# Kernel tuning notes

Hardware: AMD Instinct MI355X
Metric: run time of the kernel (lower is better)

## Reference

```python
import jax, jax.numpy as jnp
import numpy as np

B, N, C = 16, 32768, 3
PRE, POST, IOU_THRESH = 4096, 512, 0.7


def setup_inputs() -> dict:
    key = jax.random.key(0)
    k1, k2, k3, k4 = jax.random.split(key, 4)
    centers = jax.random.uniform(k1, (B, N, 3), minval=0.0, maxval=70.0)
    sizes = jax.random.uniform(k2, (B, N, 3), minval=1.0, maxval=5.0)
    ry = jax.random.uniform(k3, (B, N, 1), minval=-np.pi, maxval=np.pi)
    batch_box_preds = jnp.concatenate([centers, sizes, ry], axis=-1)  # (B,N,7)
    batch_cls_preds = jax.random.uniform(k4, (B, N, C))  # normalized class scores
    return {"batch_box_preds": batch_box_preds, "batch_cls_preds": batch_cls_preds}


def _nms_single(boxes, scores):
    """Greedy class-agnostic NMS for one sample.
    boxes: (N,7) [x,y,z,dx,dy,dz,ry]; scores: (N,).
    Returns selected indices into the original N boxes and a validity mask,
    both of fixed length POST (padded).
    BEV IoU uses axis-aligned footprints (x,y,dx,dy)."""
    top_s, top_i = jax.lax.top_k(scores, PRE)  # pre-maxsize filtering by score
    tb = boxes[top_i]  # (PRE,7)
    x1 = tb[:, 0] - tb[:, 3] * 0.5
    x2 = tb[:, 0] + tb[:, 3] * 0.5
    y1 = tb[:, 1] - tb[:, 4] * 0.5
    y2 = tb[:, 1] + tb[:, 4] * 0.5
    area = (x2 - x1) * (y2 - y1)

    def step(active, _):
        ms = jnp.where(active, top_s, -jnp.inf)
        j = jnp.argmax(ms)
        valid = active[j]
        ix = jnp.clip(jnp.minimum(x2, x2[j]) - jnp.maximum(x1, x1[j]), 0.0)
        iy = jnp.clip(jnp.minimum(y2, y2[j]) - jnp.maximum(y1, y1[j]), 0.0)
        inter = ix * iy
        iou = inter / (area + area[j] - inter + 1e-8)
        # suppress overlapping boxes (j suppresses itself, iou==1)
        active = active & jnp.where(valid, iou < IOU_THRESH, True)
        return active, (jnp.where(valid, top_i[j], 0), valid)

    active0 = jnp.ones(PRE, dtype=bool)
    _, (sel_idx, sel_valid) = jax.lax.scan(step, active0, None, length=POST)
    return sel_idx, sel_valid


def reference(batch_box_preds, batch_cls_preds):
    # cur_roi_scores, cur_roi_labels = torch.max(cls_preds, dim=1)
    scores = jnp.max(batch_cls_preds, axis=-1)          # (B,N)
    labels = jnp.argmax(batch_cls_preds, axis=-1)       # (B,N)
    sel_idx, sel_valid = jax.vmap(_nms_single)(batch_box_preds, scores)  # (B,POST)
    gather = jax.vmap(lambda a, i: a[i])
    rois = jnp.where(sel_valid[..., None], gather(batch_box_preds, sel_idx), 0.0)  # (B,POST,7)
    roi_scores = jnp.where(sel_valid, gather(scores, sel_idx), 0.0)                # (B,POST)
    roi_labels = jnp.where(sel_valid, gather(labels, sel_idx), 0) + 1              # (B,POST), pad -> 1 as in torch code
    return rois, roi_scores, roi_labels
```

## Files before the change

kernel.cpp:

```cpp
#include <hip/hip_runtime.h>
#include <stdint.h>

#define BATCH 16
#define NBOX  32768
#define PRE   4096
#define POST  512

typedef unsigned long long u64;
typedef unsigned int u32;

__device__ inline u64 shfl64(u64 v, int src) {
    int lo = __shfl((int)(v & 0xffffffffULL), src);
    int hi = __shfl((int)(v >> 32), src);
    return ((u64)(u32)hi << 32) | (u32)lo;
}

__global__ __launch_bounds__(1024) void k_sortkeys4096(const float* __restrict__ cls,
                                                       u64* __restrict__ out) {
    __shared__ u64 s[PRE];
    int g = blockIdx.x;
    u64* dst = out + (size_t)g * PRE;
    int tid = threadIdx.x;
    for (int i = tid; i < PRE; i += 1024) {
        int idx = g * PRE + i;
        const float* c = cls + (size_t)idx * 3;
        float sc = fmaxf(fmaxf(c[0], c[1]), c[2]);
        u32 sb = __float_as_uint(sc);
        s[i] = ((u64)(~sb) << 32) | (u32)(idx & (NBOX - 1));
    }
    for (int k = 2; k <= PRE; k <<= 1) {
        for (int jj = k >> 1; jj > 0; jj >>= 1) {
            __syncthreads();
            for (int p = tid; p < PRE / 2; p += 1024) {
                int i = 2 * p - (p & (jj - 1));
                int l = i + jj;
                bool asc = ((i & k) == 0);
                u64 a = s[i], b = s[l];
                if ((a > b) == asc) { s[i] = b; s[l] = a; }
            }
        }
    }
    __syncthreads();
    for (int i = tid; i < PRE; i += 1024) dst[i] = s[i];
}

__global__ __launch_bounds__(1024) void k_merge(const u64* __restrict__ in,
                                                u64* __restrict__ out, int npairs) {
    __shared__ u64 s[PRE];
    int b = blockIdx.x / npairs, p = blockIdx.x % npairs;
    const u64* A  = in + ((size_t)b * npairs * 2 + (size_t)p * 2) * PRE;
    const u64* Bp = A + PRE;
    u64* dst = out + ((size_t)b * npairs + p) * PRE;
    int tid = threadIdx.x;
    for (int i = tid; i < PRE; i += 1024) {
        u64 a = A[i], bb = Bp[PRE - 1 - i];
        s[i] = a < bb ? a : bb;
    }
    for (int jj = PRE / 2; jj > 0; jj >>= 1) {
        __syncthreads();
        for (int p2 = tid; p2 < PRE / 2; p2 += 1024) {
            int i = 2 * p2 - (p2 & (jj - 1));
            int l = i + jj;
            u64 a = s[i], bb = s[l];
            if (a > bb) { s[i] = bb; s[l] = a; }
        }
    }
    __syncthreads();
    for (int i = tid; i < PRE; i += 1024) dst[i] = s[i];
}

__global__ __launch_bounds__(256) void k_coords(const u64* __restrict__ topkeys,
                                                const float* __restrict__ boxes,
                                                float* __restrict__ cx1,
                                                float* __restrict__ cy1,
                                                float* __restrict__ cx2,
                                                float* __restrict__ cy2,
                                                float* __restrict__ car,
                                                u64* __restrict__ flags) {
    int g = blockIdx.x * 256 + threadIdx.x;
    if (g < BATCH * 64) flags[g] = 0ULL;
    int b = g >> 12;
    u64 key = topkeys[g];
    int n = (int)(key & 0xffffffffULL);
    const float* bp = boxes + ((size_t)b * NBOX + n) * 7;
    float cx = bp[0], cy = bp[1], dx = bp[3], dy = bp[4];
    float hx = __fmul_rn(dx, 0.5f), hy = __fmul_rn(dy, 0.5f);
    float x1 = __fsub_rn(cx, hx), x2 = __fadd_rn(cx, hx);
    float y1 = __fsub_rn(cy, hy), y2 = __fadd_rn(cy, hy);
    cx1[g] = x1; cy1[g] = y1; cx2[g] = x2; cy2[g] = y2;
    car[g] = __fmul_rn(__fsub_rn(x2, x1), __fsub_rn(y2, y1));
}

__global__ __launch_bounds__(256) void k_iou(const float* __restrict__ cx1,
                                             const float* __restrict__ cy1,
                                             const float* __restrict__ cx2,
                                             const float* __restrict__ cy2,
                                             const float* __restrict__ car,
                                             u64* __restrict__ maskp,
                                             u64* __restrict__ flags) {
    __shared__ float s1[64], s2[64], s3[64], s4[64], s5[64];
    int b = blockIdx.y;
    int t = blockIdx.x, blk = 0;
    while (t >= 64 - blk) { t -= 64 - blk; ++blk; }
    int wd = blk + t;
    size_t base = (size_t)b * PRE;
    int tid = threadIdx.x;
    if (tid < 64) {
        int i = blk * 64 + tid;
        s1[tid] = cx1[base + i]; s2[tid] = cy1[base + i];
        s3[tid] = cx2[base + i]; s4[tid] = cy2[base + i];
        s5[tid] = car[base + i];
    }
    __syncthreads();
    int w = tid >> 6, lane = tid & 63;
    int j = wd * 64 + lane;
    float jx1 = cx1[base + j], jy1 = cy1[base + j];
    float jx2 = cx2[base + j], jy2 = cy2[base + j];
    float ja  = car[base + j];
    const double M = (double)0.7f - 0x1p-25;
    u64 wavebits = 0;
    int r0 = w * 16;
    #pragma unroll 4
    for (int r = 0; r < 16; ++r) {
        int i = blk * 64 + r0 + r;
        float rx1 = s1[r0 + r], ry1 = s2[r0 + r];
        float rx2 = s3[r0 + r], ry2 = s4[r0 + r], ra = s5[r0 + r];
        float ix = fmaxf(__fsub_rn(fminf(jx2, rx2), fmaxf(jx1, rx1)), 0.0f);
        float iy = fmaxf(__fsub_rn(fminf(jy2, ry2), fmaxf(jy1, ry1)), 0.0f);
        float inter = __fmul_rn(ix, iy);
        bool cand = (j > i) && (inter > 0.0f);
        u64 m = 0;
        if (__ballot(cand)) {
            float ssum = __fadd_rn(ja, ra);
            float d    = __fsub_rn(ssum, inter);
            float q    = __fadd_rn(d, 1e-8f);
            bool sup = cand && ((double)inter > M * (double)q);
            m = __ballot(sup);
        }
        if (lane == 0) maskp[((base + i) << 6) + wd] = m;
        if (m) wavebits |= 1ULL << (r0 + r);
    }
    if (lane == 0 && wavebits)
        atomicOr((unsigned long long*)&flags[b * 64 + blk], wavebits);
}

__global__ __launch_bounds__(256) void k_walk(const u64* __restrict__ maskp,
                                              const u64* __restrict__ flagbits,
                                              const u64* __restrict__ topkeys,
                                              const float* __restrict__ boxes,
                                              const float* __restrict__ cls,
                                              float* __restrict__ out) {
    __shared__ int ssel[POST];
    __shared__ int scnt;
    int b = blockIdx.x;
    int tid = threadIdx.x;
    const u64* keys = topkeys + (size_t)b * PRE;

    if (tid < 64) {
        int lane = tid;
        u64 act = ~0ULL;
        u64 nzf = flagbits[b * 64 + lane];
        int cnt = 0;
        while (true) {
            u64 bal = __ballot(act != 0ULL);
            if (!bal) break;
            int fw = __ffsll(bal) - 1;
            u64 wsel = shfl64(act, fw);
            int i = (fw << 6) + __ffsll(wsel) - 1;
            if (lane == 0) ssel[cnt] = i;
            cnt++;
            if (cnt == POST) break;
            if (lane == fw) act &= ~(1ULL << (i & 63));
            u64 fword = shfl64(nzf, fw);
            if ((fword >> (i & 63)) & 1ULL) {
                u64 row = maskp[(((size_t)b * PRE + i) << 6) + lane];
                if (lane >= fw) act &= ~row;
            }
        }
        if (lane == 0) scnt = cnt;
    }
    __syncthreads();
    int cnt = scnt;
    for (int k = tid; k < POST; k += 256) if (k >= cnt) ssel[k] = -1;
    __syncthreads();

    const int R1 = BATCH * POST * 7;
    const int R2 = R1 + BATCH * POST;
    for (int k = tid; k < POST; k += 256) {
        int j = ssel[k];
        float* ro = out + ((size_t)b * POST + k) * 7;
        float score = 0.0f, labelf = 1.0f;
        if (j >= 0) {
            u64 key = keys[j];
            int n = (int)(key & 0xffffffffULL);
            const float* bp = boxes + ((size_t)b * NBOX + n) * 7;
            #pragma unroll
            for (int c = 0; c < 7; ++c) ro[c] = bp[c];
            score = __uint_as_float(~(u32)(key >> 32));
            const float* cp = cls + ((size_t)b * NBOX + n) * 3;
            float c0 = cp[0], c1 = cp[1], c2 = cp[2];
            int lab = 0; float best = c0;
            if (c1 > best) { best = c1; lab = 1; }
            if (c2 > best) { lab = 2; }
            labelf = (float)(lab + 1);
        } else {
            #pragma unroll
            for (int c = 0; c < 7; ++c) ro[c] = 0.0f;
        }
        out[R1 + b * POST + k] = score;
        out[R2 + b * POST + k] = labelf;
    }
}

__global__ __launch_bounds__(1024) void k_nms(const u64* __restrict__ topkeys,
                                              const float* __restrict__ boxes,
                                              const float* __restrict__ cls,
                                              float* __restrict__ out) {
    __shared__ float sx1[PRE], sy1[PRE], sx2[PRE], sy2[PRE], sarea[PRE];
    __shared__ int   sorig[PRE];
    __shared__ u64   smask[PRE / 64];
    __shared__ int   ssel[POST];
    __shared__ int   scur;
    int b = blockIdx.x;
    int tid = threadIdx.x;
    const u64* keys = topkeys + (size_t)b * PRE;

    for (int i = tid; i < PRE; i += 1024) {
        u64 key = keys[i];
        int n = (int)(key & 0xffffffffULL);
        sorig[i] = n;
        const float* bp = boxes + ((size_t)b * NBOX + n) * 7;
        float cx = bp[0], cy = bp[1], dx = bp[3], dy = bp[4];
        float hx = __fmul_rn(dx, 0.5f), hy = __fmul_rn(dy, 0.5f);
        float x1 = __fsub_rn(cx, hx), x2 = __fadd_rn(cx, hx);
        float y1 = __fsub_rn(cy, hy), y2 = __fadd_rn(cy, hy);
        sx1[i] = x1; sx2[i] = x2; sy1[i] = y1; sy2[i] = y2;
        sarea[i] = __fmul_rn(__fsub_rn(x2, x1), __fsub_rn(y2, y1));
    }
    if (tid < PRE / 64) smask[tid] = ~0ULL;
    __syncthreads();

    int lane = tid & 63;
    int wv   = tid >> 6;
    for (int r = 0; r < POST; ++r) {
        if (tid < 64) {
            u64 w = smask[lane];
            u64 nz = __ballot(w != 0ULL);
            int j = -1;
            if (nz) {
                int fw = __ffsll(nz) - 1;
                u64 wf = shfl64(w, fw);
                j = (fw << 6) + __ffsll(wf) - 1;
            }
            if (lane == 0) { scur = j; ssel[r] = j; }
        }
        __syncthreads();
        int j = scur;
        if (j < 0) {
            for (int k = r + tid; k < POST; k += 1024) ssel[k] = -1;
            __syncthreads();
            break;
        }
        float x1j = sx1[j], x2j = sx2[j], y1j = sy1[j], y2j = sy2[j], aj = sarea[j];
        for (int wd = wv * 4; wd < wv * 4 + 4; ++wd) {
            u64 m = smask[wd];
            if (m == 0ULL) continue;
            int i = (wd << 6) + lane;
            float ix = fmaxf(__fsub_rn(fminf(sx2[i], x2j), fmaxf(sx1[i], x1j)), 0.0f);
            float iy = fmaxf(__fsub_rn(fminf(sy2[i], y2j), fmaxf(sy1[i], y1j)), 0.0f);
            float inter = __fmul_rn(ix, iy);
            float denom = __fadd_rn(__fsub_rn(__fadd_rn(sarea[i], aj), inter), 1e-8f);
            float iou = __fdiv_rn(inter, denom);
            u64 clr = __ballot(!(iou < 0.7f));
            if (lane == 0) smask[wd] = m & ~clr;
        }
        __syncthreads();
    }

    const int R1 = BATCH * POST * 7;
    const int R2 = R1 + BATCH * POST;
    for (int k = tid; k < POST; k += 1024) {
        int j = ssel[k];
        float* ro = out + ((size_t)b * POST + k) * 7;
        float score = 0.0f, labelf = 1.0f;
        if (j >= 0) {
            int n = sorig[j];
            const float* bp = boxes + ((size_t)b * NBOX + n) * 7;
            #pragma unroll
            for (int c = 0; c < 7; ++c) ro[c] = bp[c];
            u64 key = keys[j];
            score = __uint_as_float(~(u32)(key >> 32));
            const float* cp = cls + ((size_t)b * NBOX + n) * 3;
            float c0 = cp[0], c1 = cp[1], c2 = cp[2];
            int lab = 0; float best = c0;
            if (c1 > best) { best = c1; lab = 1; }
            if (c2 > best) { lab = 2; }
            labelf = (float)(lab + 1);
        } else {
            #pragma unroll
            for (int c = 0; c < 7; ++c) ro[c] = 0.0f;
        }
        out[R1 + b * POST + k] = score;
        out[R2 + b * POST + k] = labelf;
    }
}

extern "C" void kernel_launch(void* const* d_in, const int* in_sizes, int n_in,
                              void* d_out, int out_size, void* d_ws, size_t ws_size,
                              hipStream_t stream) {
    const float* boxes = (const float*)d_in[0];
    const float* cls   = (const float*)d_in[1];
    float* out = (float*)d_out;

    char* ws = (char*)d_ws;
    u64*   keysA = (u64*)(ws + 0);
    u64*   keysB = (u64*)(ws + 4194304);
    float* cx1   = (float*)(ws + 8388608);
    float* cy1   = (float*)(ws + 8650752);
    float* cx2   = (float*)(ws + 8912896);
    float* cy2   = (float*)(ws + 9175040);
    float* car   = (float*)(ws + 9437184);
    u64*   flags = (u64*)(ws + 9699328);
    u64*   maskp = (u64*)(ws + 9707520);
    const size_t NEED = 9707520 + (size_t)BATCH * PRE * 64 * 8;

    k_sortkeys4096<<<BATCH * 8, 1024, 0, stream>>>(cls, keysB);
    k_merge<<<BATCH * 4, 1024, 0, stream>>>(keysB, keysA, 4);
    k_merge<<<BATCH * 2, 1024, 0, stream>>>(keysA, keysB, 2);

    if (ws_size >= NEED) {
        k_merge<<<BATCH, 1024, 0, stream>>>(keysB, keysA, 1);
        k_coords<<<(BATCH * PRE) / 256, 256, 0, stream>>>(keysA, boxes,
                                                          cx1, cy1, cx2, cy2, car, flags);
        k_iou<<<dim3(2080, BATCH), 256, 0, stream>>>(cx1, cy1, cx2, cy2, car,
                                                     maskp, flags);
        k_walk<<<BATCH, 256, 0, stream>>>(maskp, flags, keysA, boxes, cls, out);
    } else {
        k_merge<<<BATCH, 1024, 0, stream>>>(keysB, keysA, 1);
        k_nms<<<BATCH, 1024, 0, stream>>>(keysA, boxes, cls, out);
    }
}
```

Before: 312.2 us.

## Replace bitonic merge with merge-path merge, pad sort smem, simplify IoU candidate test

The bitonic merge kernels, which need log2(4096) compare-exchange passes each with a block barrier, are replaced by a merge-path merge. Each of 256 threads binary-searches its diagonal, then sequentially emits 16 outputs. The local bitonic sort pads its shared-memory index every 16 entries to reduce LDS bank conflicts on 64-bit accesses. In k_iou, the j>i check is applied only on diagonal tiles, since off-diagonal tiles always satisfy it. The merge-path version trades barriers for divergent sequential loads and a smaller block size.

```diff
diff --git a/kernel.cpp b/kernel.cpp
--- a/kernel.cpp
+++ b/kernel.cpp
@@ -6,6 +6,8 @@
 #define PRE   4096
 #define POST  512
 
+#define PADIDX(i) ((i) + ((i) >> 4))
+
 typedef unsigned long long u64;
 typedef unsigned int u32;
 
@@ -17,7 +19,7 @@
 
 __global__ __launch_bounds__(1024) void k_sortkeys4096(const float* __restrict__ cls,
                                                        u64* __restrict__ out) {
-    __shared__ u64 s[PRE];
+    __shared__ u64 s[PRE + (PRE >> 4)];
     int g = blockIdx.x;
     u64* dst = out + (size_t)g * PRE;
     int tid = threadIdx.x;
@@ -26,7 +28,7 @@
         const float* c = cls + (size_t)idx * 3;
         float sc = fmaxf(fmaxf(c[0], c[1]), c[2]);
         u32 sb = __float_as_uint(sc);
-        s[i] = ((u64)(~sb) << 32) | (u32)(idx & (NBOX - 1));
+        s[PADIDX(i)] = ((u64)(~sb) << 32) | (u32)(idx & (NBOX - 1));
     }
     for (int k = 2; k <= PRE; k <<= 1) {
         for (int jj = k >> 1; jj > 0; jj >>= 1) {
@@ -35,38 +37,45 @@
                 int i = 2 * p - (p & (jj - 1));
                 int l = i + jj;
                 bool asc = ((i & k) == 0);
-                u64 a = s[i], b = s[l];
-                if ((a > b) == asc) { s[i] = b; s[l] = a; }
+                u64 a = s[PADIDX(i)], b = s[PADIDX(l)];
+                if ((a > b) == asc) { s[PADIDX(i)] = b; s[PADIDX(l)] = a; }
             }
         }
     }
     __syncthreads();
-    for (int i = tid; i < PRE; i += 1024) dst[i] = s[i];
-}
-
-__global__ __launch_bounds__(1024) void k_merge(const u64* __restrict__ in,
-                                                u64* __restrict__ out, int npairs) {
-    __shared__ u64 s[PRE];
+    for (int i = tid; i < PRE; i += 1024) dst[i] = s[PADIDX(i)];
+}
+
+__global__ __launch_bounds__(256) void k_mergepath(const u64* __restrict__ in,
+                                                   u64* __restrict__ out, int npairs) {
+    __shared__ u64 sA[PRE], sB[PRE];
     int b = blockIdx.x / npairs, p = blockIdx.x % npairs;
     const u64* A  = in + ((size_t)b * npairs * 2 + (size_t)p * 2) * PRE;
     const u64* Bp = A + PRE;
     u64* dst = out + ((size_t)b * npairs + p) * PRE;
     int tid = threadIdx.x;
-    for (int i = tid; i < PRE; i += 1024) {
-        u64 a = A[i], bb = Bp[PRE - 1 - i];
-        s[i] = a < bb ? a : bb;
-    }
-    for (int jj = PRE / 2; jj > 0; jj >>= 1) {
-        __syncthreads();
-        for (int p2 = tid; p2 < PRE / 2; p2 += 1024) {
-            int i = 2 * p2 - (p2 & (jj - 1));
-            int l = i + jj;
-            u64 a = s[i], bb = s[l];
-            if (a > bb) { s[i] = bb; s[l] = a; }
-        }
-    }
-    __syncthreads();
-    for (int i = tid; i < PRE; i += 1024) dst[i] = s[i];
+    for (int i = tid; i < PRE; i += 256) { sA[i] = A[i]; sB[i] = Bp[i]; }
+    __syncthreads();
+    int d = tid * 16;
+    int lo = d > PRE ? d - PRE : 0;
+    int hi = d < PRE ? d : PRE;
+    while (lo < hi) {
+        int mid = (lo + hi) >> 1;
+        if (sA[mid] < sB[d - 1 - mid]) lo = mid + 1; else hi = mid;
+    }
+    int a = lo, bi = d - lo;
+    u64 av = a  < PRE ? sA[a]  : ~0ULL;
+    u64 bv = bi < PRE ? sB[bi] : ~0ULL;
+    u64 res[16];
+    #pragma unroll
+    for (int q = 0; q < 16; ++q) {
+        bool ta = av < bv;
+        res[q] = ta ? av : bv;
+        if (ta) { ++a;  av = a  < PRE ? sA[a]  : ~0ULL; }
+        else    { ++bi; bv = bi < PRE ? sB[bi] : ~0ULL; }
+    }
+    #pragma unroll
+    for (int q = 0; q < 16; ++q) dst[d + q] = res[q];
 }
 
 __global__ __launch_bounds__(256) void k_coords(const u64* __restrict__ topkeys,
@@ -103,6 +112,7 @@
     int t = blockIdx.x, blk = 0;
     while (t >= 64 - blk) { t -= 64 - blk; ++blk; }
     int wd = blk + t;
+    bool diag = (wd == blk);
     size_t base = (size_t)b * PRE;
     int tid = threadIdx.x;
     if (tid < 64) {
@@ -128,7 +138,7 @@
         float ix = fmaxf(__fsub_rn(fminf(jx2, rx2), fmaxf(jx1, rx1)), 0.0f);
         float iy = fmaxf(__fsub_rn(fminf(jy2, ry2), fmaxf(jy1, ry1)), 0.0f);
         float inter = __fmul_rn(ix, iy);
-        bool cand = (j > i) && (inter > 0.0f);
+        bool cand = (inter > 0.0f) && (!diag || j > i);
         u64 m = 0;
         if (__ballot(cand)) {
             float ssum = __fadd_rn(ja, ra);
@@ -325,18 +335,17 @@
     const size_t NEED = 9707520 + (size_t)BATCH * PRE * 64 * 8;
 
     k_sortkeys4096<<<BATCH * 8, 1024, 0, stream>>>(cls, keysB);
-    k_merge<<<BATCH * 4, 1024, 0, stream>>>(keysB, keysA, 4);
-    k_merge<<<BATCH * 2, 1024, 0, stream>>>(keysA, keysB, 2);
+    k_mergepath<<<BATCH * 4, 256, 0, stream>>>(keysB, keysA, 4);
+    k_mergepath<<<BATCH * 2, 256, 0, stream>>>(keysA, keysB, 2);
+    k_mergepath<<<BATCH, 256, 0, stream>>>(keysB, keysA, 1);
 
     if (ws_size >= NEED) {
-        k_merge<<<BATCH, 1024, 0, stream>>>(keysB, keysA, 1);
         k_coords<<<(BATCH * PRE) / 256, 256, 0, stream>>>(keysA, boxes,
                                                           cx1, cy1, cx2, cy2, car, flags);
         k_iou<<<dim3(2080, BATCH), 256, 0, stream>>>(cx1, cy1, cx2, cy2, car,
                                                      maskp, flags);
         k_walk<<<BATCH, 256, 0, stream>>>(maskp, flags, keysA, boxes, cls, out);
     } else {
-        k_merge<<<BATCH, 1024, 0, stream>>>(keysB, keysA, 1);
         k_nms<<<BATCH, 1024, 0, stream>>>(keysA, boxes, cls, out);
     }
 }
```

Measured after the change: 328.3 us. 1.05x slower.
